# Performance work log

Measured on AMD Instinct MI355X. Metric: run time of the kernel, lower is better.

The kernel has to match this reference:

```python
import jax, jax.numpy as jnp
import numpy as np

B, N, H = 32, 1024, 256
ALPHA = 0.2  # leaky relu slope
NEG_INF = -1e12


def setup_inputs() -> dict:
    key = jax.random.key(0)
    k1, k2, k3, k4, k5, k6 = jax.random.split(key, 6)
    inp = jax.random.normal(k1, (B, N, H), dtype=jnp.float32)
    A = (jax.random.uniform(k2, (B, N, N)) < 0.05).astype(jnp.float32)
    l = jnp.sort(jax.random.randint(k3, (B, 2), 0, N), axis=1)
    # xavier-uniform(gain=1.414) approximated; exact init values are irrelevant for correctness
    lim_w = 1.414 * np.sqrt(6.0 / (H + H))
    W_i = jax.random.uniform(k4, (H, H), minval=-lim_w, maxval=lim_w, dtype=jnp.float32)
    W_c = jax.random.uniform(k5, (H, H), minval=-lim_w, maxval=lim_w, dtype=jnp.float32)
    lim_a = 1.414 * np.sqrt(6.0 / (2 * H + 1))
    a = jax.random.uniform(k6, (2 * H, 1), minval=-lim_a, maxval=lim_a, dtype=jnp.float32)
    return {"inp": inp, "A": A, "l": l, "W_i": W_i, "W_c": W_c, "a": a}


def reference(inp, A, l, W_i, W_c, a):
    # eval mode: dropout is identity (training=False)
    n = inp.shape[1]
    h = inp.shape[2]
    Wh_i = jnp.einsum('bnh,he->bne', inp, W_i)
    Wh_c = jnp.einsum('bnh,he->bne', inp, W_c)
    # vectorized replacement of the per-batch Wh[index][i:j] = Wh_i[index][i:j] loop
    idx = jnp.arange(n)
    sel = (idx[None, :] >= l[:, 0:1]) & (idx[None, :] < l[:, 1:2])  # [B,N]
    Wh = jnp.where(sel[:, :, None], Wh_i, Wh_c)
    # additive attention scores
    Wh1 = Wh @ a[:h, :]  # [B,N,1]
    Wh2 = Wh @ a[h:, :]  # [B,N,1]
    A_ = A + jnp.eye(n, dtype=A.dtype)
    e = jax.nn.leaky_relu((Wh1 + jnp.swapaxes(Wh2, 1, 2)) * A_, ALPHA)
    att = jnp.where(A_ > 0, e, NEG_INF)
    att = jax.nn.softmax(att, axis=2)
    h_prime = jnp.einsum('bnm,bme->bne', att, Wh)
    return jax.nn.elu(h_prime)  # concat=True
```

## Files before the change

kernel.cpp:

```cpp
#include <hip/hip_runtime.h>
#include <hip/hip_bf16.h>
#include <stdint.h>

#define B_ 32
#define N_ 1024
#define H_ 256
#define PF_PITCH 520

typedef short bf16x8 __attribute__((ext_vector_type(8)));
typedef float floatx4 __attribute__((ext_vector_type(4)));

__device__ inline unsigned short f2bs(float x) {
    __hip_bfloat16 h = __float2bfloat16(x);
    return __builtin_bit_cast(unsigned short, h);
}

__global__ __launch_bounds__(256)
void k_uvec(const float* __restrict__ Wi, const float* __restrict__ Wc,
            const float* __restrict__ a, float* __restrict__ U) {
    int k = blockIdx.x;
    int t = threadIdx.x;
    float wi = Wi[k * H_ + t];
    float wc = Wc[k * H_ + t];
    float a1 = a[t], a2 = a[H_ + t];
    float p0 = wi * a1, p1 = wc * a1, p2 = wi * a2, p3 = wc * a2;
    for (int off = 32; off; off >>= 1) {
        p0 += __shfl_xor(p0, off);
        p1 += __shfl_xor(p1, off);
        p2 += __shfl_xor(p2, off);
        p3 += __shfl_xor(p3, off);
    }
    __shared__ float red[4][4];
    int w = t >> 6;
    if ((t & 63) == 0) { red[w][0] = p0; red[w][1] = p1; red[w][2] = p2; red[w][3] = p3; }
    __syncthreads();
    if (t == 0) {
        U[0 * H_ + k] = red[0][0] + red[1][0] + red[2][0] + red[3][0];
        U[1 * H_ + k] = red[0][1] + red[1][1] + red[2][1] + red[3][1];
        U[2 * H_ + k] = red[0][2] + red[1][2] + red[2][2] + red[3][2];
        U[3 * H_ + k] = red[0][3] + red[1][3] + red[2][3] + red[3][3];
    }
}

__global__ __launch_bounds__(256)
void k_prep(const float* __restrict__ Wi, const float* __restrict__ Wc,
            unsigned short* __restrict__ WtFi, unsigned short* __restrict__ WtFc) {
    __shared__ float tile[64][65];
    int mat = blockIdx.x >> 4;
    int tr = ((blockIdx.x >> 2) & 3) * 64;
    int tc = (blockIdx.x & 3) * 64;
    const float* W = mat ? Wc : Wi;
    unsigned short* WtF = mat ? WtFc : WtFi;
    int t = threadIdx.x;
    int rr = t >> 2, c4 = (t & 3) * 16;
    const float* src = W + (size_t)(tr + rr) * H_ + tc + c4;
#pragma unroll
    for (int j = 0; j < 4; ++j) {
        float4 v = *reinterpret_cast<const float4*>(src + j * 4);
        tile[rr][c4 + 4 * j + 0] = v.x;
        tile[rr][c4 + 4 * j + 1] = v.y;
        tile[rr][c4 + 4 * j + 2] = v.z;
        tile[rr][c4 + 4 * j + 3] = v.w;
    }
    __syncthreads();
#pragma unroll
    for (int h = 0; h < 2; ++h) {
        int s = h * 256 + t;
        int ksl = s >> 8;
        int cl  = (s >> 6) & 3;
        int ll  = s & 63;
        int m16v = ll & 15, quadv = ll >> 4;
        int nloc = cl * 16 + m16v;
        int kb = ksl * 32 + quadv * 8;
        unsigned int pk[4];
#pragma unroll
        for (int jj = 0; jj < 4; ++jj) {
            unsigned short lo = f2bs(tile[kb + 2 * jj][nloc]);
            unsigned short hi = f2bs(tile[kb + 2 * jj + 1][nloc]);
            pk[jj] = (unsigned int)lo | ((unsigned int)hi << 16);
        }
        int ksg = (tr >> 5) + ksl;
        int cg  = (tc >> 4) + cl;
        *reinterpret_cast<uint4*>(WtF + ((size_t)(ksg * 16 + cg) * 64 + ll) * 8) =
            *reinterpret_cast<uint4*>(pk);
    }
}

__global__ __launch_bounds__(256)
void k_gemm(const float* __restrict__ inp, const int* __restrict__ l,
            const unsigned short* __restrict__ WtFi, const unsigned short* __restrict__ WtFc,
            unsigned short* __restrict__ WhF, const float* __restrict__ U,
            float* __restrict__ Wh1, float* __restrict__ Wh2) {
    __shared__ unsigned short bbuf[2][4096];
    int blk = blockIdx.x;
    int b  = blk >> 5;
    int r0 = ((blk >> 1) & 15) * 64;
    int n0 = (blk & 1) * 128;
    int t = threadIdx.x;
    int w = t >> 6;
    int lane = t & 63;
    int quad = lane >> 4, m16 = lane & 15;
    int rowb = r0 + w * 16;

    int l0 = l[2 * b], l1 = l[2 * b + 1];
    bool allI = (l0 <= r0) && (r0 + 64 <= l1);
    bool allC = (l1 <= r0) || (l0 >= r0 + 64);
    int npass = (allI || allC) ? 1 : 2;

    int row = rowb + m16;
    bool sel = (row >= l0) && (row < l1);
    const float* xrow = inp + ((size_t)(b * N_ + row)) * H_;
    const float* u1 = U + (sel ? 0 : H_);
    const float* u2 = U + 2 * H_ + (sel ? 0 : H_);
    bool doWh = (n0 == 0);
    float d1 = 0.f, d2 = 0.f;

    unsigned short* fb = WhF + (size_t)b * (N_ * H_);
    int cb = n0 >> 4;

    int j0 = rowb + quad * 4;
    int ksO = j0 >> 5;
    int laneF = m16 + 16 * ((j0 & 31) >> 3);
    int jj0 = j0 & 7;

    for (int pass = 0; pass < npass; ++pass) {
        const unsigned short* WtF =
            (npass == 1) ? (allI ? WtFi : WtFc) : (pass == 0 ? WtFi : WtFc);
        const unsigned short* gbase = WtF + cb * 512;

        floatx4 acc[8];
#pragma unroll
        for (int c = 0; c < 8; ++c) acc[c] = (floatx4){0.f, 0.f, 0.f, 0.f};

        {
            uint4 v0 = *reinterpret_cast<const uint4*>(gbase + (size_t)t * 8);
            uint4 v1 = *reinterpret_cast<const uint4*>(gbase + (size_t)(256 + t) * 8);
            *reinterpret_cast<uint4*>(&bbuf[0][t * 8]) = v0;
            *reinterpret_cast<uint4*>(&bbuf[0][(256 + t) * 8]) = v1;
        }
        for (int ks = 0; ks < 8; ++ks) {
            __syncthreads();
            uint4 v0, v1;
            if (ks < 7) {
                v0 = *reinterpret_cast<const uint4*>(gbase + (size_t)(ks + 1) * 8192 + t * 8);
                v1 = *reinterpret_cast<const uint4*>(gbase + (size_t)(ks + 1) * 8192 + (256 + t) * 8);
            }
            const float4 xa = *reinterpret_cast<const float4*>(xrow + ks * 32 + quad * 8);
            const float4 xb = *reinterpret_cast<const float4*>(xrow + ks * 32 + quad * 8 + 4);
            if (pass == 0 && doWh) {
                const float4 ua = *reinterpret_cast<const float4*>(u1 + ks * 32 + quad * 8);
                const float4 ub = *reinterpret_cast<const float4*>(u1 + ks * 32 + quad * 8 + 4);
                const float4 va = *reinterpret_cast<const float4*>(u2 + ks * 32 + quad * 8);
                const float4 vb = *reinterpret_cast<const float4*>(u2 + ks * 32 + quad * 8 + 4);
                d1 += xa.x * ua.x + xa.y * ua.y + xa.z * ua.z + xa.w * ua.w
                    + xb.x * ub.x + xb.y * ub.y + xb.z * ub.z + xb.w * ub.w;
                d2 += xa.x * va.x + xa.y * va.y + xa.z * va.z + xa.w * va.w
                    + xb.x * vb.x + xb.y * vb.y + xb.z * vb.z + xb.w * vb.w;
            }
            unsigned int pk0 = (unsigned int)f2bs(xa.x) | ((unsigned int)f2bs(xa.y) << 16);
            unsigned int pk1 = (unsigned int)f2bs(xa.z) | ((unsigned int)f2bs(xa.w) << 16);
            unsigned int pk2 = (unsigned int)f2bs(xb.x) | ((unsigned int)f2bs(xb.y) << 16);
            unsigned int pk3 = (unsigned int)f2bs(xb.z) | ((unsigned int)f2bs(xb.w) << 16);
            uint4 apk = {pk0, pk1, pk2, pk3};
            bf16x8 af = __builtin_bit_cast(bf16x8, apk);

            const unsigned short* bptr = &bbuf[ks & 1][lane * 8];
#pragma unroll
            for (int c = 0; c < 8; ++c) {
                bf16x8 bfr = *reinterpret_cast<const bf16x8*>(bptr + c * 512);
                acc[c] = __builtin_amdgcn_mfma_f32_16x16x32_bf16(af, bfr, acc[c], 0, 0, 0);
            }
            if (ks < 7) {
                *reinterpret_cast<uint4*>(&bbuf[(ks + 1) & 1][t * 8]) = v0;
                *reinterpret_cast<uint4*>(&bbuf[(ks + 1) & 1][(256 + t) * 8]) = v1;
            }
        }
        __syncthreads();

#pragma unroll
        for (int c = 0; c < 8; ++c) {
            size_t base = ((size_t)((ksO * 16 + cb + c) * 64) + laneF) * 8 + jj0;
            if (npass == 1) {
                unsigned int lo = (unsigned int)f2bs(acc[c][0]) | ((unsigned int)f2bs(acc[c][1]) << 16);
                unsigned int hi = (unsigned int)f2bs(acc[c][2]) | ((unsigned int)f2bs(acc[c][3]) << 16);
                uint2 v = {lo, hi};
                *reinterpret_cast<uint2*>(fb + base) = v;
            } else {
                bool want[4]; bool all = true, none = true;
#pragma unroll
                for (int r = 0; r < 4; ++r) {
                    int j = j0 + r;
                    bool s2 = (j >= l0) && (j < l1);
                    want[r] = (pass == 0) ? s2 : !s2;
                    all = all && want[r]; none = none && !want[r];
                }
                if (all) {
                    unsigned int lo = (unsigned int)f2bs(acc[c][0]) | ((unsigned int)f2bs(acc[c][1]) << 16);
                    unsigned int hi = (unsigned int)f2bs(acc[c][2]) | ((unsigned int)f2bs(acc[c][3]) << 16);
                    uint2 v = {lo, hi};
                    *reinterpret_cast<uint2*>(fb + base) = v;
                } else if (!none) {
#pragma unroll
                    for (int r = 0; r < 4; ++r)
                        if (want[r]) fb[base + r] = f2bs(acc[c][r]);
                }
            }
        }
    }

    if (doWh) {
        d1 += __shfl_xor(d1, 16); d1 += __shfl_xor(d1, 32);
        d2 += __shfl_xor(d2, 16); d2 += __shfl_xor(d2, 32);
        if (quad == 0) {
            Wh1[b * N_ + rowb + m16] = d1;
            Wh2[b * N_ + rowb + m16] = d2;
        }
    }
}

__global__ __launch_bounds__(256, 4)
void k_attn(const float* __restrict__ A, const float* __restrict__ Wh1,
            const float* __restrict__ Wh2, const unsigned short* __restrict__ WhF,
            float* __restrict__ out) {
    __shared__ unsigned short pfrag[32 * PF_PITCH];
    int t = threadIdx.x, w = t >> 6, lane = t & 63;
    int bi = blockIdx.x;
    int b = (bi & 7) * 4 + (bi >> 8);
    int tile = (bi >> 3) & 31;
    int rowbase = tile * 32;

    int ksl = lane >> 3;
    int q2 = (lane >> 1) & 3;
    int jj0 = (lane & 1) * 4;

    const unsigned short* WB = WhF + (size_t)b * (N_ * H_);
    int rs = (lane ^ ((lane >> 3) & 7)) * 8;
    unsigned short oneb = f2bs(1.0f);
    bf16x8 bones = {(short)oneb, (short)oneb, (short)oneb, (short)oneb,
                    (short)oneb, (short)oneb, (short)oneb, (short)oneb};
    int quad = lane >> 4, m16 = lane & 15;

    for (int tt = 0; tt < 2; ++tt) {
        if (tt) __syncthreads();

        const float* Wh2b = Wh2 + b * N_;
        float4 w2v[4];
#pragma unroll
        for (int ch = 0; ch < 4; ++ch)
            w2v[ch] = *reinterpret_cast<const float4*>(Wh2b + ch * 256 + lane * 4);

        float4 av[4][4];
        float wh1v[4];
#pragma unroll
        for (int q = 0; q < 4; ++q) {
            int i = rowbase + tt * 16 + w * 4 + q;
            wh1v[q] = Wh1[b * N_ + i];
            const float* Arow = A + ((size_t)(b * N_ + i)) * N_;
#pragma unroll
            for (int ch = 0; ch < 4; ++ch)
                av[q][ch] = *reinterpret_cast<const float4*>(Arow + ch * 256 + lane * 4);
        }
#pragma unroll
        for (int q = 0; q < 4; ++q) {
            int m = w * 4 + q;
            int i = rowbase + tt * 16 + m;
            float wh1 = wh1v[q];
            int s = m + 16 * q2;
            int sw = s ^ ((s >> 3) & 7);
            int sls = sw * 8 + jj0;
#pragma unroll
            for (int ch = 0; ch < 4; ++ch) {
                float4 avv = av[q][ch];
                if ((i >> 2) == (ch * 64 + lane)) ((float*)&avv)[i & 3] += 1.0f;
                float aa[4] = {avv.x, avv.y, avv.z, avv.w};
                float ww[4] = {w2v[ch].x, w2v[ch].y, w2v[ch].z, w2v[ch].w};
                float p[4];
#pragma unroll
                for (int c = 0; c < 4; ++c) {
                    float e  = (wh1 + ww[c]) * aa[c];
                    float lv = fmaxf(e, 0.2f * e);
                    p[c] = aa[c] > 0.f ? __expf(lv) : 0.f;
                }
                unsigned int lo = (unsigned int)f2bs(p[0]) | ((unsigned int)f2bs(p[1]) << 16);
                unsigned int hi = (unsigned int)f2bs(p[2]) | ((unsigned int)f2bs(p[3]) << 16);
                uint2 v = {lo, hi};
                int ks = ch * 8 + ksl;
                *reinterpret_cast<uint2*>(pfrag + ks * PF_PITCH + sls) = v;
            }
        }
        __syncthreads();

        floatx4 acc[4], sum;
        sum = (floatx4){0.f, 0.f, 0.f, 0.f};
#pragma unroll
        for (int cc = 0; cc < 4; ++cc)
            acc[cc] = (floatx4){0.f, 0.f, 0.f, 0.f};
#pragma unroll 2
        for (int ks = 0; ks < 32; ++ks) {
            bf16x8 af = *reinterpret_cast<const bf16x8*>(pfrag + ks * PF_PITCH + rs);
            sum = __builtin_amdgcn_mfma_f32_16x16x32_bf16(af, bones, sum, 0, 0, 0);
#pragma unroll
            for (int cc = 0; cc < 4; ++cc) {
                int c = w * 4 + cc;
                bf16x8 bfv = *reinterpret_cast<const bf16x8*>(
                    WB + ((size_t)((ks * 16 + c) * 64 + lane)) * 8);
                acc[cc] = __builtin_amdgcn_mfma_f32_16x16x32_bf16(af, bfv, acc[cc], 0, 0, 0);
            }
        }

        float inv[4];
#pragma unroll
        for (int r = 0; r < 4; ++r)
            inv[r] = 1.0f / sum[r];
#pragma unroll
        for (int cc = 0; cc < 4; ++cc) {
            int col = (w * 4 + cc) * 16 + m16;
#pragma unroll
            for (int r = 0; r < 4; ++r) {
                int m = quad * 4 + r;
                float v0 = acc[cc][r] * inv[r];
                v0 = v0 > 0.f ? v0 : __expf(v0) - 1.0f;
                out[((size_t)(b * N_ + rowbase + tt * 16 + m)) * H_ + col] = v0;
            }
        }
    }
}

extern "C" void kernel_launch(void* const* d_in, const int* in_sizes, int n_in,
                              void* d_out, int out_size, void* d_ws, size_t ws_size,
                              hipStream_t stream) {
    const float* inp = (const float*)d_in[0];
    const float* A   = (const float*)d_in[1];
    const int*   l   = (const int*)d_in[2];
    const float* Wi  = (const float*)d_in[3];
    const float* Wc  = (const float*)d_in[4];
    const float* a   = (const float*)d_in[5];
    float* out = (float*)d_out;

    char* ws = (char*)d_ws;
    size_t off = 0;
    unsigned short* WhF  = (unsigned short*)(ws + off); off += (size_t)B_ * N_ * H_ * 2;
    float* Wh1 = (float*)(ws + off); off += (size_t)B_ * N_ * 4;
    float* Wh2 = (float*)(ws + off); off += (size_t)B_ * N_ * 4;
    float* U   = (float*)(ws + off); off += 4 * H_ * 4;
    unsigned short* WtFi = (unsigned short*)(ws + off); off += (size_t)H_ * H_ * 2;
    unsigned short* WtFc = (unsigned short*)(ws + off); off += (size_t)H_ * H_ * 2;

    k_uvec<<<H_, 256, 0, stream>>>(Wi, Wc, a, U);
    k_prep<<<32, 256, 0, stream>>>(Wi, Wc, WtFi, WtFc);
    k_gemm<<<B_ * 16 * 2, 256, 0, stream>>>(inp, l, WtFi, WtFc, WhF, U, Wh1, Wh2);
    k_attn<<<B_ * (N_ / 32), 256, 0, stream>>>(A, Wh1, Wh2, WhF, out);
}
```

Baseline: 287.3 us.

## Enlarge attention tile to 64 rows with 512 threads and reuse WhF fragments

The attention kernel now processes 64 query rows per block with 8 waves. It builds all four 16-row probability tiles in shared memory before a single barrier. Each wave loads its WhF B-fragments once per k-step and reuses them across four row tiles, instead of reloading them for each of two 16-row passes. Row sums are now computed with shuffle reductions during the exp step rather than by an extra MFMA against a ones vector. The cost is more shared memory (about 133KB dynamic), more accumulator registers and fewer blocks per CU.

```diff
diff --git a/kernel.cpp b/kernel.cpp
--- a/kernel.cpp
+++ b/kernel.cpp
@@ -6,6 +6,8 @@
 #define N_ 1024
 #define H_ 256
 #define PF_PITCH 520
+#define PF_HALF (32 * PF_PITCH)
+#define K_ATTN_SMEM (4 * PF_HALF * 2 + 64 * 4)
 
 typedef short bf16x8 __attribute__((ext_vector_type(8)));
 typedef float floatx4 __attribute__((ext_vector_type(4)));
@@ -218,56 +220,52 @@
     }
 }
 
-__global__ __launch_bounds__(256, 4)
+__global__ __launch_bounds__(512, 2)
 void k_attn(const float* __restrict__ A, const float* __restrict__ Wh1,
             const float* __restrict__ Wh2, const unsigned short* __restrict__ WhF,
             float* __restrict__ out) {
-    __shared__ unsigned short pfrag[32 * PF_PITCH];
+    extern __shared__ unsigned short smem[];
+    unsigned short* pfrag = smem;
+    float* rsum = reinterpret_cast<float*>(smem + 4 * PF_HALF);
     int t = threadIdx.x, w = t >> 6, lane = t & 63;
     int bi = blockIdx.x;
-    int b = (bi & 7) * 4 + (bi >> 8);
-    int tile = (bi >> 3) & 31;
-    int rowbase = tile * 32;
+    int b    = (bi & 7) * 4 + (bi >> 7);
+    int tile = (bi >> 3) & 15;
+    int rowbase = tile * 64;
 
     int ksl = lane >> 3;
-    int q2 = (lane >> 1) & 3;
+    int q2  = (lane >> 1) & 3;
     int jj0 = (lane & 1) * 4;
 
-    const unsigned short* WB = WhF + (size_t)b * (N_ * H_);
-    int rs = (lane ^ ((lane >> 3) & 7)) * 8;
-    unsigned short oneb = f2bs(1.0f);
-    bf16x8 bones = {(short)oneb, (short)oneb, (short)oneb, (short)oneb,
-                    (short)oneb, (short)oneb, (short)oneb, (short)oneb};
-    int quad = lane >> 4, m16 = lane & 15;
-
-    for (int tt = 0; tt < 2; ++tt) {
-        if (tt) __syncthreads();
-
-        const float* Wh2b = Wh2 + b * N_;
-        float4 w2v[4];
-#pragma unroll
-        for (int ch = 0; ch < 4; ++ch)
-            w2v[ch] = *reinterpret_cast<const float4*>(Wh2b + ch * 256 + lane * 4);
-
-        float4 av[4][4];
-        float wh1v[4];
-#pragma unroll
-        for (int q = 0; q < 4; ++q) {
-            int i = rowbase + tt * 16 + w * 4 + q;
+    const float* Wh2b = Wh2 + b * N_;
+    float4 w2v[4];
+#pragma unroll
+    for (int ch = 0; ch < 4; ++ch)
+        w2v[ch] = *reinterpret_cast<const float4*>(Wh2b + ch * 256 + lane * 4);
+
+#pragma unroll
+    for (int h = 0; h < 4; ++h) {
+        float4 av[2][4];
+        float wh1v[2];
+#pragma unroll
+        for (int q = 0; q < 2; ++q) {
+            int i = rowbase + h * 16 + w * 2 + q;
             wh1v[q] = Wh1[b * N_ + i];
             const float* Arow = A + ((size_t)(b * N_ + i)) * N_;
 #pragma unroll
             for (int ch = 0; ch < 4; ++ch)
                 av[q][ch] = *reinterpret_cast<const float4*>(Arow + ch * 256 + lane * 4);
         }
-#pragma unroll
-        for (int q = 0; q < 4; ++q) {
-            int m = w * 4 + q;
-            int i = rowbase + tt * 16 + m;
+        unsigned short* pf = pfrag + h * PF_HALF;
+#pragma unroll
+        for (int q = 0; q < 2; ++q) {
+            int m = w * 2 + q;
+            int i = rowbase + h * 16 + m;
             float wh1 = wh1v[q];
-            int s = m + 16 * q2;
+            int s  = m + 16 * q2;
             int sw = s ^ ((s >> 3) & 7);
             int sls = sw * 8 + jj0;
+            float rp = 0.f;
 #pragma unroll
             for (int ch = 0; ch < 4; ++ch) {
                 float4 avv = av[q][ch];
@@ -281,46 +279,61 @@
                     float lv = fmaxf(e, 0.2f * e);
                     p[c] = aa[c] > 0.f ? __expf(lv) : 0.f;
                 }
+                rp += (p[0] + p[1]) + (p[2] + p[3]);
                 unsigned int lo = (unsigned int)f2bs(p[0]) | ((unsigned int)f2bs(p[1]) << 16);
                 unsigned int hi = (unsigned int)f2bs(p[2]) | ((unsigned int)f2bs(p[3]) << 16);
                 uint2 v = {lo, hi};
                 int ks = ch * 8 + ksl;
-                *reinterpret_cast<uint2*>(pfrag + ks * PF_PITCH + sls) = v;
-            }
-        }
-        __syncthreads();
-
-        floatx4 acc[4], sum;
-        sum = (floatx4){0.f, 0.f, 0.f, 0.f};
-#pragma unroll
-        for (int cc = 0; cc < 4; ++cc)
-            acc[cc] = (floatx4){0.f, 0.f, 0.f, 0.f};
+                *reinterpret_cast<uint2*>(pf + ks * PF_PITCH + sls) = v;
+            }
+            for (int off = 32; off; off >>= 1) rp += __shfl_xor(rp, off);
+            if (lane == 0) rsum[h * 16 + m] = rp;
+        }
+    }
+    __syncthreads();
+
+    const unsigned short* WB = WhF + (size_t)b * (N_ * H_);
+    int rs = (lane ^ ((lane >> 3) & 7)) * 8;
+    floatx4 acc[4][2];
+#pragma unroll
+    for (int h = 0; h < 4; ++h)
+#pragma unroll
+        for (int cc = 0; cc < 2; ++cc)
+            acc[h][cc] = (floatx4){0.f, 0.f, 0.f, 0.f};
+
 #pragma unroll 2
-        for (int ks = 0; ks < 32; ++ks) {
-            bf16x8 af = *reinterpret_cast<const bf16x8*>(pfrag + ks * PF_PITCH + rs);
-            sum = __builtin_amdgcn_mfma_f32_16x16x32_bf16(af, bones, sum, 0, 0, 0);
-#pragma unroll
-            for (int cc = 0; cc < 4; ++cc) {
-                int c = w * 4 + cc;
-                bf16x8 bfv = *reinterpret_cast<const bf16x8*>(
-                    WB + ((size_t)((ks * 16 + c) * 64 + lane)) * 8);
-                acc[cc] = __builtin_amdgcn_mfma_f32_16x16x32_bf16(af, bfv, acc[cc], 0, 0, 0);
-            }
-        }
-
-        float inv[4];
-#pragma unroll
-        for (int r = 0; r < 4; ++r)
-            inv[r] = 1.0f / sum[r];
-#pragma unroll
-        for (int cc = 0; cc < 4; ++cc) {
-            int col = (w * 4 + cc) * 16 + m16;
+    for (int ks = 0; ks < 32; ++ks) {
+        bf16x8 bfv[2];
+#pragma unroll
+        for (int cc = 0; cc < 2; ++cc) {
+            int c = w * 2 + cc;
+            bfv[cc] = *reinterpret_cast<const bf16x8*>(
+                WB + ((size_t)((ks * 16 + c) * 64 + lane)) * 8);
+        }
+        bf16x8 af[4];
+#pragma unroll
+        for (int h = 0; h < 4; ++h)
+            af[h] = *reinterpret_cast<const bf16x8*>(pfrag + h * PF_HALF + ks * PF_PITCH + rs);
+#pragma unroll
+        for (int h = 0; h < 4; ++h)
+#pragma unroll
+            for (int cc = 0; cc < 2; ++cc)
+                acc[h][cc] = __builtin_amdgcn_mfma_f32_16x16x32_bf16(af[h], bfv[cc], acc[h][cc], 0, 0, 0);
+    }
+
+    int quad = lane >> 4, m16 = lane & 15;
+#pragma unroll
+    for (int h = 0; h < 4; ++h) {
+        float4 rv = *reinterpret_cast<const float4*>(&rsum[h * 16 + quad * 4]);
+        float inv[4] = {1.0f / rv.x, 1.0f / rv.y, 1.0f / rv.z, 1.0f / rv.w};
+#pragma unroll
+        for (int cc = 0; cc < 2; ++cc) {
+            int col = (w * 2 + cc) * 16 + m16;
 #pragma unroll
             for (int r = 0; r < 4; ++r) {
-                int m = quad * 4 + r;
-                float v0 = acc[cc][r] * inv[r];
+                float v0 = acc[h][cc][r] * inv[r];
                 v0 = v0 > 0.f ? v0 : __expf(v0) - 1.0f;
-                out[((size_t)(b * N_ + rowbase + tt * 16 + m)) * H_ + col] = v0;
+                out[((size_t)(b * N_ + rowbase + h * 16 + quad * 4 + r)) * H_ + col] = v0;
             }
         }
     }
@@ -346,8 +359,15 @@
     unsigned short* WtFi = (unsigned short*)(ws + off); off += (size_t)H_ * H_ * 2;
     unsigned short* WtFc = (unsigned short*)(ws + off); off += (size_t)H_ * H_ * 2;
 
+    static bool s_attr = false;
+    if (!s_attr) {
+        hipFuncSetAttribute(reinterpret_cast<const void*>(k_attn),
+                            hipFuncAttributeMaxDynamicSharedMemorySize, K_ATTN_SMEM);
+        s_attr = true;
+    }
+
     k_uvec<<<H_, 256, 0, stream>>>(Wi, Wc, a, U);
     k_prep<<<32, 256, 0, stream>>>(Wi, Wc, WtFi, WtFc);
     k_gemm<<<B_ * 16 * 2, 256, 0, stream>>>(inp, l, WtFi, WtFc, WhF, U, Wh1, Wh2);
-    k_attn<<<B_ * (N_ / 32), 256, 0, stream>>>(A, Wh1, Wh2, WhF, out);
-}
+    k_attn<<<B_ * (N_ / 64), 512, K_ATTN_SMEM, stream>>>(A, Wh1, Wh2, WhF, out);
+}
```

Measured after the change: 298.4 us. +3.9%, slower.
